# Kernel optimization log

Measured on AMD Instinct MI355X. Metric: run time of the kernel, lower is better.

Reference implementation:

```python
import jax, jax.numpy as jnp
import numpy as np
from jax import lax

B, S, L, E, H, V = 32, 64, 256, 64, 64, 6000


def setup_inputs() -> dict:
    key = jax.random.key(0)
    ks = jax.random.split(key, 8)
    inp = {
        "ids": jax.random.randint(ks[0], (B, S, L), 0, V, dtype=jnp.int32),
        "embed_table": jax.random.normal(ks[1], (V, E), jnp.float32) * 0.05,
        "Wk_f": jax.random.normal(ks[2], (E, 4 * H), jnp.float32) * 0.05,
        "Wr_f": jax.random.normal(ks[3], (H, 4 * H), jnp.float32) * 0.05,
        "b_f": jnp.zeros((4 * H,), jnp.float32),
        "Wk_b": jax.random.normal(ks[4], (E, 4 * H), jnp.float32) * 0.05,
        "Wr_b": jax.random.normal(ks[5], (H, 4 * H), jnp.float32) * 0.05,
        "b_b": jnp.zeros((4 * H,), jnp.float32),
    }
    return inp


def _lstm(xs, Wk, Wr, b):
    # xs: [L, N, E] -> hidden states [L, N, H]; Keras LSTM gate order i,f,c,o
    N = xs.shape[1]
    Hh = Wr.shape[0]
    pre = jnp.einsum('lne,eg->lng', xs, Wk) + b  # input projection once, outside scan

    def step(carry, zt):
        h, c = carry
        z = zt + h @ Wr
        i, f, g, o = jnp.split(z, 4, axis=-1)
        i = jax.nn.sigmoid(i)
        f = jax.nn.sigmoid(f)
        g = jnp.tanh(g)
        o = jax.nn.sigmoid(o)
        c = f * c + i * g
        h = o * jnp.tanh(c)
        return (h, c), h

    h0 = jnp.zeros((N, Hh), xs.dtype)
    _, hs = lax.scan(step, (h0, h0), pre)
    return hs


def reference(ids, embed_table, Wk_f, Wr_f, b_f, Wk_b, Wr_b, b_b):
    b, s, l = ids.shape
    e = embed_table.shape[1]
    h = Wr_f.shape[0]
    x = embed_table[ids]                      # [B,S,L,E]
    xs = x.reshape(b * s, l, e).transpose(1, 0, 2)  # [L, B*S, E]
    h_fwd = _lstm(xs, Wk_f, Wr_f, b_f)              # [L, N, H]
    h_bwd = _lstm(xs[::-1], Wk_b, Wr_b, b_b)[::-1]  # [L, N, H]
    out = jnp.concatenate([h_fwd, h_bwd], axis=-1)  # [L, N, 2H]
    return out.transpose(1, 0, 2).reshape(b, s, l, 2 * h)
```

## Files before the change

kernel.cpp:

```cpp
#include <hip/hip_runtime.h>

#define LL 256
#define EE 64
#define HH 64
#define GG 256
#define VV 6000
#define NSEQ 16
#define ROWP 72
#define VBLK 375

typedef __bf16 bf16_t;
typedef bf16_t bf16x8 __attribute__((ext_vector_type(8)));
typedef float  f32x4  __attribute__((ext_vector_type(4)));

union BfPack {
    unsigned short u[8];
    bf16x8 v;
};

__device__ __forceinline__ unsigned short f2bf(float f) {
    return __builtin_bit_cast(unsigned short, (__bf16)f);
}

#define LOG2E 1.44269504088896340736f

__device__ __forceinline__ float sigm(float x) {
    float e = __builtin_amdgcn_exp2f(-LOG2E * x);
    return __builtin_amdgcn_rcpf(1.0f + e);
}
__device__ __forceinline__ float tanh_fast(float x) {
    float e = __builtin_amdgcn_exp2f((2.0f * LOG2E) * x);
    return 1.0f - 2.0f * __builtin_amdgcn_rcpf(e + 1.0f);
}

#define LGKM_BARRIER() asm volatile("s_waitcnt lgkmcnt(0)\n\ts_barrier" ::: "memory")

__global__ __launch_bounds__(256)
void embed_pre_kernel(const float* __restrict__ embed,
                      const float* __restrict__ Wk_f, const float* __restrict__ b_f,
                      const float* __restrict__ Wk_b, const float* __restrict__ b_b,
                      float* __restrict__ pre)
{
    const int bid = blockIdx.x;
    const int dir = bid / VBLK;
    const int v0  = (bid % VBLK) * 16;
    const float* Wk = dir ? Wk_b : Wk_f;
    const float* bv = dir ? b_b  : b_f;
    float* dst = pre + (size_t)dir * VV * GG;

    const int tid = threadIdx.x;
    const int r   = tid >> 4;
    const int cg  = tid & 15;

    __shared__ float sW[16][GG];
    __shared__ float sE[16][17];

    float acc[16];
    #pragma unroll
    for (int k = 0; k < 16; ++k) acc[k] = 0.f;

    for (int ec = 0; ec < 4; ++ec) {
        {
            int er = tid >> 4;
            int c0 = (tid & 15) * 16;
            const float* src = &Wk[(size_t)(ec * 16 + er) * GG + c0];
            *(float4*)&sW[er][c0 + 0]  = *(const float4*)(src + 0);
            *(float4*)&sW[er][c0 + 4]  = *(const float4*)(src + 4);
            *(float4*)&sW[er][c0 + 8]  = *(const float4*)(src + 8);
            *(float4*)&sW[er][c0 + 12] = *(const float4*)(src + 12);
            sE[er][tid & 15] = embed[(size_t)(v0 + er) * EE + ec * 16 + (tid & 15)];
        }
        __syncthreads();
        #pragma unroll
        for (int e = 0; e < 16; ++e) {
            float xe = sE[r][e];
            #pragma unroll
            for (int k = 0; k < 16; ++k)
                acc[k] += xe * sW[e][k * 16 + cg];
        }
        __syncthreads();
    }
    #pragma unroll
    for (int k = 0; k < 16; ++k) {
        int g = k * 16 + cg;
        int pos = ((g >> 4) & 3) * 64 + (g & 15) * 4 + (g >> 6);
        dst[(size_t)(v0 + r) * GG + pos] = acc[k] + bv[g];
    }
}

__global__ __launch_bounds__(256, 1)
void bilstm_mfma(const int* __restrict__ ids,
                 const float* __restrict__ Wr_f, const float* __restrict__ Wr_b,
                 const float* __restrict__ pre,
                 float* __restrict__ out)
{
    const int dir = blockIdx.x >> 7;
    const int grp = blockIdx.x & 127;
    const int n0  = grp * NSEQ;
    const int tid  = threadIdx.x;
    const int w    = tid >> 6;
    const int lane = tid & 63;
    const int l15  = lane & 15;
    const int quad = lane >> 4;
    const int j    = w * 16 + l15;

    const float* Wr = dir ? Wr_b : Wr_f;
    const float* preT = pre + (size_t)dir * VV * GG;
    const int coff = w * 64 + l15 * 4;

    __shared__ __align__(16) short s_h[2][NSEQ][ROWP];
    __shared__ int s_ids[NSEQ][LL + 1];

    for (int p = tid; p < NSEQ * LL; p += 256) {
        int m = p >> 8, t = p & 255;
        s_ids[m][t] = ids[(size_t)(n0 + m) * LL + t];
    }
    for (int p = tid; p < 2 * NSEQ * ROWP; p += 256)
        (&s_h[0][0][0])[p] = 0;

    __syncthreads();

    bf16x8 bfrag[4][2];
    #pragma unroll
    for (int tt = 0; tt < 4; ++tt) {
        int g = tt * 64 + j;
        #pragma unroll
        for (int kc = 0; kc < 2; ++kc) {
            BfPack pk;
            #pragma unroll
            for (int e = 0; e < 8; ++e) {
                int kg = kc * 32 + quad * 8 + e;
                pk.u[e] = f2bf(Wr[(size_t)kg * GG + g]);
            }
            bfrag[tt][kc] = pk.v;
        }
    }

    f32x4 PA[4], PB[4];
    {
        int t0 = dir ? (LL - 1) : 0;
        int t1 = dir ? (LL - 2) : 1;
        #pragma unroll
        for (int r = 0; r < 4; ++r) {
            PA[r] = *(const f32x4*)&preT[(size_t)s_ids[quad * 4 + r][t0] * GG + coff];
            PB[r] = *(const f32x4*)&preT[(size_t)s_ids[quad * 4 + r][t1] * GG + coff];
        }
    }

    float c[4] = {0.f, 0.f, 0.f, 0.f};

    const int tstep = dir ? -(2 * HH) : (2 * HH);
    float* optr[4];
    {
        const int t0 = dir ? (LL - 1) : 0;
        #pragma unroll
        for (int r = 0; r < 4; ++r)
            optr[r] = out + ((size_t)(n0 + quad * 4 + r) * LL + t0) * (2 * HH) + dir * HH + j;
    }

    auto do_step = [&](int ts, f32x4 (&P)[4]) {
        const int rb = ts & 1, wb = (ts + 1) & 1;

        f32x4 cIn[4];
        #pragma unroll
        for (int tt = 0; tt < 4; ++tt)
            cIn[tt] = (f32x4){P[0][tt], P[1][tt], P[2][tt], P[3][tt]};

        if (ts + 2 < LL) {
            int tn = dir ? (LL - 3 - ts) : (ts + 2);
            #pragma unroll
            for (int r = 0; r < 4; ++r)
                P[r] = *(const f32x4*)&preT[(size_t)s_ids[quad * 4 + r][tn] * GG + coff];
        }

        bf16x8 ah0 = *(const bf16x8*)&s_h[rb][l15][quad * 8];
        bf16x8 ah1 = *(const bf16x8*)&s_h[rb][l15][32 + quad * 8];

        f32x4 acc[4];
        #pragma unroll
        for (int tt = 0; tt < 4; ++tt) {
            f32x4 a = __builtin_amdgcn_mfma_f32_16x16x32_bf16(ah0, bfrag[tt][0], cIn[tt], 0, 0, 0);
            acc[tt]  = __builtin_amdgcn_mfma_f32_16x16x32_bf16(ah1, bfrag[tt][1], a, 0, 0, 0);
        }

        #pragma unroll
        for (int r = 0; r < 4; ++r) {
            float ig = sigm(acc[0][r]);
            float fg = sigm(acc[1][r]);
            float gg = tanh_fast(acc[2][r]);
            float og = sigm(acc[3][r]);
            c[r] = fg * c[r] + ig * gg;
            float hh = og * tanh_fast(c[r]);
            __builtin_nontemporal_store(hh, optr[r]);
            optr[r] += tstep;
            s_h[wb][quad * 4 + r][j] = (short)f2bf(hh);
        }

        LGKM_BARRIER();
    };

    for (int ts = 0; ts < LL; ts += 2) {
        do_step(ts,     PA);
        do_step(ts + 1, PB);
    }
}

extern "C" void kernel_launch(void* const* d_in, const int* in_sizes, int n_in,
                              void* d_out, int out_size, void* d_ws, size_t ws_size,
                              hipStream_t stream) {
    const int*   ids   = (const int*)d_in[0];
    const float* embed = (const float*)d_in[1];
    const float* Wk_f  = (const float*)d_in[2];
    const float* Wr_f  = (const float*)d_in[3];
    const float* b_f   = (const float*)d_in[4];
    const float* Wk_b  = (const float*)d_in[5];
    const float* Wr_b  = (const float*)d_in[6];
    const float* b_b   = (const float*)d_in[7];
    float* out = (float*)d_out;
    float* pre = (float*)d_ws;

    embed_pre_kernel<<<dim3(2 * VBLK), dim3(256), 0, stream>>>(
        embed, Wk_f, b_f, Wk_b, b_b, pre);

    bilstm_mfma<<<dim3(256), dim3(256), 0, stream>>>(ids, Wr_f, Wr_b, pre, out);
}
```

Baseline: 473.5 us.

## Store precomputed gate table in bf16 and reorder per-step loads

New measurement: 405.5 us. 1.17x faster.

```diff
diff --git a/kernel.cpp b/kernel.cpp
--- a/kernel.cpp
+++ b/kernel.cpp
@@ -39,14 +39,14 @@
 void embed_pre_kernel(const float* __restrict__ embed,
                       const float* __restrict__ Wk_f, const float* __restrict__ b_f,
                       const float* __restrict__ Wk_b, const float* __restrict__ b_b,
-                      float* __restrict__ pre)
+                      unsigned short* __restrict__ pre)
 {
     const int bid = blockIdx.x;
     const int dir = bid / VBLK;
     const int v0  = (bid % VBLK) * 16;
     const float* Wk = dir ? Wk_b : Wk_f;
     const float* bv = dir ? b_b  : b_f;
-    float* dst = pre + (size_t)dir * VV * GG;
+    unsigned short* dst = pre + (size_t)dir * VV * GG;
 
     const int tid = threadIdx.x;
     const int r   = tid >> 4;
@@ -81,17 +81,20 @@
         __syncthreads();
     }
     #pragma unroll
-    for (int k = 0; k < 16; ++k) {
-        int g = k * 16 + cg;
-        int pos = ((g >> 4) & 3) * 64 + (g & 15) * 4 + (g >> 6);
-        dst[(size_t)(v0 + r) * GG + pos] = acc[k] + bv[g];
+    for (int a = 0; a < 4; ++a) {
+        ushort4 pk;
+        pk.x = f2bf(acc[a]      + bv[(a)      * 16 + cg]);
+        pk.y = f2bf(acc[a + 4]  + bv[(a + 4)  * 16 + cg]);
+        pk.z = f2bf(acc[a + 8]  + bv[(a + 8)  * 16 + cg]);
+        pk.w = f2bf(acc[a + 12] + bv[(a + 12) * 16 + cg]);
+        *(ushort4*)&dst[(size_t)(v0 + r) * GG + a * 64 + cg * 4] = pk;
     }
 }
 
 __global__ __launch_bounds__(256, 1)
 void bilstm_mfma(const int* __restrict__ ids,
                  const float* __restrict__ Wr_f, const float* __restrict__ Wr_b,
-                 const float* __restrict__ pre,
+                 const unsigned short* __restrict__ pre,
                  float* __restrict__ out)
 {
     const int dir = blockIdx.x >> 7;
@@ -105,7 +108,7 @@
     const int j    = w * 16 + l15;
 
     const float* Wr = dir ? Wr_b : Wr_f;
-    const float* preT = pre + (size_t)dir * VV * GG;
+    const unsigned short* preT = pre + (size_t)dir * VV * GG;
     const int coff = w * 64 + l15 * 4;
 
     __shared__ __align__(16) short s_h[2][NSEQ][ROWP];
@@ -136,14 +139,14 @@
         }
     }
 
-    f32x4 PA[4], PB[4];
+    uint2 PA[4], PB[4];
     {
         int t0 = dir ? (LL - 1) : 0;
         int t1 = dir ? (LL - 2) : 1;
         #pragma unroll
         for (int r = 0; r < 4; ++r) {
-            PA[r] = *(const f32x4*)&preT[(size_t)s_ids[quad * 4 + r][t0] * GG + coff];
-            PB[r] = *(const f32x4*)&preT[(size_t)s_ids[quad * 4 + r][t1] * GG + coff];
+            PA[r] = *(const uint2*)&preT[(size_t)s_ids[quad * 4 + r][t0] * GG + coff];
+            PB[r] = *(const uint2*)&preT[(size_t)s_ids[quad * 4 + r][t1] * GG + coff];
         }
     }
 
@@ -158,23 +161,28 @@
             optr[r] = out + ((size_t)(n0 + quad * 4 + r) * LL + t0) * (2 * HH) + dir * HH + j;
     }
 
-    auto do_step = [&](int ts, f32x4 (&P)[4]) {
+    auto do_step = [&](int ts, uint2 (&P)[4]) {
         const int rb = ts & 1, wb = (ts + 1) & 1;
 
+        bf16x8 ah0 = *(const bf16x8*)&s_h[rb][l15][quad * 8];
+        bf16x8 ah1 = *(const bf16x8*)&s_h[rb][l15][32 + quad * 8];
+
         f32x4 cIn[4];
         #pragma unroll
-        for (int tt = 0; tt < 4; ++tt)
-            cIn[tt] = (f32x4){P[0][tt], P[1][tt], P[2][tt], P[3][tt]};
-
-        if (ts + 2 < LL) {
+        for (int r = 0; r < 4; ++r) {
+            cIn[0][r] = __uint_as_float(P[r].x << 16);
+            cIn[1][r] = __uint_as_float(P[r].x & 0xffff0000u);
+            cIn[2][r] = __uint_as_float(P[r].y << 16);
+            cIn[3][r] = __uint_as_float(P[r].y & 0xffff0000u);
+        }
+
+        {
             int tn = dir ? (LL - 3 - ts) : (ts + 2);
+            tn = tn < 0 ? 0 : (tn > LL - 1 ? LL - 1 : tn);
             #pragma unroll
             for (int r = 0; r < 4; ++r)
-                P[r] = *(const f32x4*)&preT[(size_t)s_ids[quad * 4 + r][tn] * GG + coff];
-        }
-
-        bf16x8 ah0 = *(const bf16x8*)&s_h[rb][l15][quad * 8];
-        bf16x8 ah1 = *(const bf16x8*)&s_h[rb][l15][32 + quad * 8];
+                P[r] = *(const uint2*)&preT[(size_t)s_ids[quad * 4 + r][tn] * GG + coff];
+        }
 
         f32x4 acc[4];
         #pragma unroll
@@ -191,7 +199,7 @@
             float og = sigm(acc[3][r]);
             c[r] = fg * c[r] + ig * gg;
             float hh = og * tanh_fast(c[r]);
-            __builtin_nontemporal_store(hh, optr[r]);
+            *optr[r] = hh;
             optr[r] += tstep;
             s_h[wb][quad * 4 + r][j] = (short)f2bf(hh);
         }
@@ -217,7 +225,7 @@
     const float* Wr_b  = (const float*)d_in[6];
     const float* b_b   = (const float*)d_in[7];
     float* out = (float*)d_out;
-    float* pre = (float*)d_ws;
+    unsigned short* pre = (unsigned short*)d_ws;
 
     embed_pre_kernel<<<dim3(2 * VBLK), dim3(256), 0, stream>>>(
         embed, Wk_f, b_f, Wk_b, b_b, pre);
```
